# Performance work log

Hardware: AMD Instinct MI355X
Metric: run time of the kernel (lower is better)

## Reference

```python
import jax, jax.numpy as jnp
import numpy as np
import math

D_MODEL = 1024
N_HEADS = 16
HEAD_DIM = D_MODEL // N_HEADS
RANK = 128
SCALE = 1.0 / math.sqrt(HEAD_DIM)


def lowrank(x, u, v, b):
    # y = (x @ u) @ v + b : d_model -> rank -> d_model
    return jnp.einsum('bsd,dr,re->bse', x, u, v) + b


def setup_inputs() -> dict:
    key = jax.random.key(0)
    ks = jax.random.split(key, 16)
    B, S = 2, 2048
    inp = {
        'q': jax.random.normal(ks[0], (B, S, D_MODEL), jnp.float32),
        'k': jax.random.normal(ks[1], (B, S, D_MODEL), jnp.float32),
        'v': jax.random.normal(ks[2], (B, S, D_MODEL), jnp.float32),
        'mask': jnp.ones((B, S), jnp.int32),
    }
    i = 3
    for name in ('q', 'k', 'v', 'out'):
        inp[f'{name}_u'] = jax.random.normal(ks[i], (D_MODEL, RANK), jnp.float32) * 0.02
        inp[f'{name}_v'] = jax.random.normal(ks[i + 1], (RANK, D_MODEL), jnp.float32) * 0.02
        inp[f'{name}_b'] = jnp.zeros((D_MODEL,), jnp.float32)
        i += 2
    return inp


def reference(q, k, v, mask, q_u, q_v, q_b, k_u, k_v, k_b, v_u, v_v, v_b, out_u, out_v, out_b):
    B, S, _ = q.shape
    qh = lowrank(q, q_u, q_v, q_b).reshape(B, S, N_HEADS, HEAD_DIM)
    kh = lowrank(k, k_u, k_v, k_b).reshape(B, S, N_HEADS, HEAD_DIM)
    vh = lowrank(v, v_u, v_v, v_b).reshape(B, S, N_HEADS, HEAD_DIM)
    # scores: [B, H, Sq, Sk]
    scores = jnp.einsum('bqhd,bkhd->bhqk', qh, kh) * SCALE
    scores = jnp.where(mask[:, None, None, :] == 0, -1e9, scores)
    attn = jax.nn.softmax(scores, axis=-1)
    ctx = jnp.einsum('bhqk,bkhd->bqhd', attn, vh).reshape(B, S, D_MODEL)
    return lowrank(ctx, out_u, out_v, out_b)
```

## Files before the change

kernel.cpp:

```cpp
#include <hip/hip_runtime.h>
#include <hip/hip_bf16.h>
#include <stdint.h>

#define DEVI __device__ __forceinline__

typedef __attribute__((ext_vector_type(8))) __bf16 bf16x8;
typedef __attribute__((ext_vector_type(4))) float f32x4;
typedef __attribute__((ext_vector_type(4))) unsigned short us4;

DEVI unsigned short f2bf(float x) {
  union { float f; unsigned u; } v; v.f = x;
  unsigned r = v.u + 0x7FFFu + ((v.u >> 16) & 1u);
  return (unsigned short)(r >> 16);
}

DEVI f32x4 mfma16(bf16x8 a, bf16x8 b, f32x4 c) {
  return __builtin_amdgcn_mfma_f32_16x16x32_bf16(a, b, c, 0, 0, 0);
}

DEVI bf16x8 ld_frag(const unsigned short* tile, int row, int ld, int kbase, int lane) {
  const unsigned short* p = tile + row * ld + kbase + ((lane >> 4) << 2);
  union { bf16x8 f; us4 h[2]; } u;
  u.h[0] = *(const us4*)p;
  u.h[1] = *(const us4*)(p + 16);
  return u.f;
}

struct TP { const float* in[8]; unsigned short* out[8]; };

__global__ __launch_bounds__(256) void wtrans(TP p) {
  const int z = blockIdx.y;
  const int K = (z & 1) ? 128 : 1024;
  const int N = (z & 1) ? 1024 : 128;
  const int i = blockIdx.x * 256 + threadIdx.x;
  const int k = i / N, n = i % N;
  p.out[z][(size_t)n * K + k] = f2bf(p.in[z][i]);
}

struct GP {
  const void* A[3];
  const unsigned short* WT[3];
  const float* bias[3];
  void* C[3];
  float oscale[3];
};

template<bool ABF16, bool OBF16, bool BIAS>
__global__ __launch_bounds__(256)
void gemm_k(GP p, int M, int N, int K) {
  __shared__ unsigned short As[128][36];
  __shared__ unsigned short Ws[64][36];
  const int tid = threadIdx.x, lane = tid & 63, wid = tid >> 6;
  const int z = blockIdx.z;
  const int m0 = blockIdx.x * 128, n0 = blockIdx.y * 64;
  const int wm = (wid >> 1) * 64, wn = (wid & 1) * 32;
  f32x4 acc[4][2] = {};

  const int arow = tid >> 1, aseg = (tid & 1) * 16;
  const int wrow = tid >> 2, wseg = (tid & 3) * 8;
  const float* Af = (const float*)p.A[z];
  const unsigned short* Ab = (const unsigned short*)p.A[z];
  const unsigned short* Wt = p.WT[z];

  for (int k0 = 0; k0 < K; k0 += 32) {
    __syncthreads();
    {
      union { uint4 u[2]; us4 h[4]; unsigned short s[16]; } t;
      if (ABF16) {
        const unsigned short* src = Ab + (size_t)(m0 + arow) * K + k0 + aseg;
        t.u[0] = *(const uint4*)src;
        t.u[1] = *(const uint4*)(src + 8);
      } else {
        const float* src = Af + (size_t)(m0 + arow) * K + k0 + aseg;
        #pragma unroll
        for (int j = 0; j < 16; j += 4) {
          float4 f = *(const float4*)(src + j);
          t.s[j] = f2bf(f.x); t.s[j + 1] = f2bf(f.y);
          t.s[j + 2] = f2bf(f.z); t.s[j + 3] = f2bf(f.w);
        }
      }
      us4* dst = (us4*)&As[arow][aseg];
      dst[0] = t.h[0]; dst[1] = t.h[1]; dst[2] = t.h[2]; dst[3] = t.h[3];
    }
    {
      union { uint4 u; us4 h[2]; } t;
      const unsigned short* src = Wt + (size_t)(n0 + wrow) * K + k0 + wseg;
      t.u = *(const uint4*)src;
      us4* dst = (us4*)&Ws[wrow][wseg];
      dst[0] = t.h[0]; dst[1] = t.h[1];
    }
    __syncthreads();

    bf16x8 af[4], wf[2];
    #pragma unroll
    for (int mi = 0; mi < 4; mi++)
      af[mi] = ld_frag(&As[0][0], wm + mi * 16 + (lane & 15), 36, 0, lane);
    #pragma unroll
    for (int ni = 0; ni < 2; ni++)
      wf[ni] = ld_frag(&Ws[0][0], wn + ni * 16 + (lane & 15), 36, 0, lane);
    #pragma unroll
    for (int mi = 0; mi < 4; mi++)
      #pragma unroll
      for (int ni = 0; ni < 2; ni++)
        acc[mi][ni] = mfma16(af[mi], wf[ni], acc[mi][ni]);
  }

  const float os = p.oscale[z];
  #pragma unroll
  for (int ni = 0; ni < 2; ni++) {
    const int col = n0 + wn + ni * 16 + (lane & 15);
    const float bv = BIAS ? p.bias[z][col] : 0.0f;
    #pragma unroll
    for (int mi = 0; mi < 4; mi++)
      #pragma unroll
      for (int r = 0; r < 4; r++) {
        const int row = m0 + wm + mi * 16 + ((lane >> 4) << 2) + r;
        float vv = (acc[mi][ni][r] + bv) * os;
        if (OBF16) ((unsigned short*)p.C[z])[(size_t)row * N + col] = f2bf(vv);
        else       ((float*)p.C[z])[(size_t)row * N + col] = vv;
      }
  }
}

__global__ __launch_bounds__(256)
void attn_k(const unsigned short* __restrict__ qh, const unsigned short* __restrict__ kh,
            const unsigned short* __restrict__ vh, const int* __restrict__ mask,
            unsigned short* __restrict__ ctx) {
  const int S = 2048, DM = 1024;
  __shared__ unsigned short Ks[64][68];
  __shared__ unsigned short VTs[64][68];
  __shared__ unsigned short Ps[4][32][68];
  __shared__ float mk[64];
  const int tid = threadIdx.x, lane = tid & 63, w = tid >> 6;
  const int b = blockIdx.z, h = blockIdx.y, q0 = blockIdx.x * 128;
  const int qbase = q0 + w * 32;

  bf16x8 qf[2][2];
  #pragma unroll
  for (int mi = 0; mi < 2; mi++)
    #pragma unroll
    for (int kk = 0; kk < 2; kk++) {
      const unsigned short* p = qh + (size_t)(b * S + qbase + mi * 16 + (lane & 15)) * DM
                                + h * 64 + kk * 32 + ((lane >> 4) << 2);
      union { bf16x8 f; us4 h4[2]; } u;
      u.h4[0] = *(const us4*)p;
      u.h4[1] = *(const us4*)(p + 16);
      qf[mi][kk] = u.f;
    }

  float mrow[2][4], lrow[2][4];
  f32x4 acc[2][4] = {};
  #pragma unroll
  for (int mi = 0; mi < 2; mi++)
    #pragma unroll
    for (int r = 0; r < 4; r++) { mrow[mi][r] = -1e30f; lrow[mi][r] = 0.f; }

  const int srow = tid >> 2, sseg = (tid & 3) * 16;

  for (int kv0 = 0; kv0 < S; kv0 += 64) {
    __syncthreads();
    {
      union { uint4 u[2]; us4 h[4]; unsigned short s[16]; } tk, tv;
      const unsigned short* ksrc = kh + (size_t)(b * S + kv0 + srow) * DM + h * 64 + sseg;
      tk.u[0] = *(const uint4*)ksrc; tk.u[1] = *(const uint4*)(ksrc + 8);
      us4* kd = (us4*)&Ks[srow][sseg];
      kd[0] = tk.h[0]; kd[1] = tk.h[1]; kd[2] = tk.h[2]; kd[3] = tk.h[3];
      const unsigned short* vsrc = vh + (size_t)(b * S + kv0 + srow) * DM + h * 64 + sseg;
      tv.u[0] = *(const uint4*)vsrc; tv.u[1] = *(const uint4*)(vsrc + 8);
      #pragma unroll
      for (int j = 0; j < 16; j++) VTs[sseg + j][srow] = tv.s[j];
      if (tid < 64) mk[tid] = (mask[b * S + kv0 + tid] == 0) ? -1e9f : 0.0f;
    }
    __syncthreads();

    f32x4 sc[2][4];
    #pragma unroll
    for (int ni = 0; ni < 4; ni++) {
      bf16x8 kf0 = ld_frag(&Ks[0][0], ni * 16 + (lane & 15), 68, 0, lane);
      bf16x8 kf1 = ld_frag(&Ks[0][0], ni * 16 + (lane & 15), 68, 32, lane);
      #pragma unroll
      for (int mi = 0; mi < 2; mi++) {
        f32x4 zz = {0.f, 0.f, 0.f, 0.f};
        zz = mfma16(qf[mi][0], kf0, zz);
        zz = mfma16(qf[mi][1], kf1, zz);
        sc[mi][ni] = zz;
      }
    }
    #pragma unroll
    for (int mi = 0; mi < 2; mi++)
      #pragma unroll
      for (int ni = 0; ni < 4; ni++) {
        float ma = mk[ni * 16 + (lane & 15)];
        sc[mi][ni] += ma;
      }

    #pragma unroll
    for (int mi = 0; mi < 2; mi++)
      #pragma unroll
      for (int r = 0; r < 4; r++) {
        float tm = fmaxf(fmaxf(sc[mi][0][r], sc[mi][1][r]), fmaxf(sc[mi][2][r], sc[mi][3][r]));
        tm = fmaxf(tm, __shfl_xor(tm, 1));
        tm = fmaxf(tm, __shfl_xor(tm, 2));
        tm = fmaxf(tm, __shfl_xor(tm, 4));
        tm = fmaxf(tm, __shfl_xor(tm, 8));
        float mnew = fmaxf(mrow[mi][r], tm);
        float alpha = __expf(mrow[mi][r] - mnew);
        mrow[mi][r] = mnew;
        float rs = 0.f;
        #pragma unroll
        for (int ni = 0; ni < 4; ni++) {
          float e = __expf(sc[mi][ni][r] - mnew);
          sc[mi][ni][r] = e;
          rs += e;
        }
        rs += __shfl_xor(rs, 1);
        rs += __shfl_xor(rs, 2);
        rs += __shfl_xor(rs, 4);
        rs += __shfl_xor(rs, 8);
        lrow[mi][r] = lrow[mi][r] * alpha + rs;
        #pragma unroll
        for (int di = 0; di < 4; di++) acc[mi][di][r] *= alpha;
      }

    #pragma unroll
    for (int mi = 0; mi < 2; mi++)
      #pragma unroll
      for (int ni = 0; ni < 4; ni++)
        #pragma unroll
        for (int r = 0; r < 4; r++)
          Ps[w][mi * 16 + ((lane >> 4) << 2) + r][ni * 16 + (lane & 15)] = f2bf(sc[mi][ni][r]);

    #pragma unroll
    for (int kk = 0; kk < 2; kk++) {
      bf16x8 pa0 = ld_frag(&Ps[w][0][0], 0 * 16 + (lane & 15), 68, kk * 32, lane);
      bf16x8 pa1 = ld_frag(&Ps[w][0][0], 1 * 16 + (lane & 15), 68, kk * 32, lane);
      #pragma unroll
      for (int di = 0; di < 4; di++) {
        bf16x8 vb = ld_frag(&VTs[0][0], di * 16 + (lane & 15), 68, kk * 32, lane);
        acc[0][di] = mfma16(pa0, vb, acc[0][di]);
        acc[1][di] = mfma16(pa1, vb, acc[1][di]);
      }
    }
  }

  #pragma unroll
  for (int mi = 0; mi < 2; mi++)
    #pragma unroll
    for (int di = 0; di < 4; di++)
      #pragma unroll
      for (int r = 0; r < 4; r++) {
        const int row = qbase + mi * 16 + ((lane >> 4) << 2) + r;
        float o = acc[mi][di][r] / lrow[mi][r];
        ctx[(size_t)(b * S + row) * DM + h * 64 + di * 16 + (lane & 15)] = f2bf(o);
      }
}

extern "C" void kernel_launch(void* const* d_in, const int* in_sizes, int n_in,
                              void* d_out, int out_size, void* d_ws, size_t ws_size,
                              hipStream_t stream) {
  const float* q = (const float*)d_in[0];
  const float* k = (const float*)d_in[1];
  const float* v = (const float*)d_in[2];
  const int* mask = (const int*)d_in[3];
  const float* wu[4] = {(const float*)d_in[4], (const float*)d_in[7],
                        (const float*)d_in[10], (const float*)d_in[13]};
  const float* wv[4] = {(const float*)d_in[5], (const float*)d_in[8],
                        (const float*)d_in[11], (const float*)d_in[14]};
  const float* wb[4] = {(const float*)d_in[6], (const float*)d_in[9],
                        (const float*)d_in[12], (const float*)d_in[15]};

  char* ws = (char*)d_ws;
  unsigned short* WT  = (unsigned short*)ws;
  unsigned short* T0  = (unsigned short*)(ws + 2097152);
  unsigned short* T1  = T0 + 524288;
  unsigned short* T2  = T1 + 524288;
  unsigned short* QH  = (unsigned short*)(ws + 2097152 + 3145728);
  unsigned short* KH  = QH + 4194304;
  unsigned short* VH  = KH + 4194304;
  unsigned short* CTX = VH + 4194304;

  TP tp;
  for (int i = 0; i < 4; i++) { tp.in[2 * i] = wu[i]; tp.in[2 * i + 1] = wv[i]; }
  for (int i = 0; i < 8; i++) tp.out[i] = WT + (size_t)i * 131072;
  wtrans<<<dim3(512, 8), 256, 0, stream>>>(tp);

  const float SCALE = 0.125f;

  GP g1 = {};
  g1.A[0] = q; g1.A[1] = k; g1.A[2] = v;
  g1.WT[0] = tp.out[0]; g1.WT[1] = tp.out[2]; g1.WT[2] = tp.out[4];
  g1.C[0] = T0; g1.C[1] = T1; g1.C[2] = T2;
  g1.oscale[0] = g1.oscale[1] = g1.oscale[2] = 1.f;
  gemm_k<false, true, false><<<dim3(32, 2, 3), 256, 0, stream>>>(g1, 4096, 128, 1024);

  GP g2 = {};
  g2.A[0] = T0; g2.A[1] = T1; g2.A[2] = T2;
  g2.WT[0] = tp.out[1]; g2.WT[1] = tp.out[3]; g2.WT[2] = tp.out[5];
  g2.bias[0] = wb[0]; g2.bias[1] = wb[1]; g2.bias[2] = wb[2];
  g2.C[0] = QH; g2.C[1] = KH; g2.C[2] = VH;
  g2.oscale[0] = SCALE; g2.oscale[1] = 1.f; g2.oscale[2] = 1.f;
  gemm_k<true, true, true><<<dim3(32, 16, 3), 256, 0, stream>>>(g2, 4096, 1024, 128);

  attn_k<<<dim3(16, 16, 2), 256, 0, stream>>>(QH, KH, VH, mask, CTX);

  GP g3 = {};
  g3.A[0] = CTX; g3.WT[0] = tp.out[6]; g3.C[0] = T0; g3.oscale[0] = 1.f;
  gemm_k<true, true, false><<<dim3(32, 2, 1), 256, 0, stream>>>(g3, 4096, 128, 1024);

  GP g4 = {};
  g4.A[0] = T0; g4.WT[0] = tp.out[7]; g4.bias[0] = wb[3];
  g4.C[0] = d_out; g4.oscale[0] = 1.f;
  gemm_k<true, false, true><<<dim3(32, 16, 1), 256, 0, stream>>>(g4, 4096, 1024, 128);
}
```

Before: 319.0 us.

## Compute transposed attention scores to keep P in registers, tile weight transpose

The attention kernel now computes S^T = K·Q^T, so each lane holds a column of scores for one query. The softmax reduction then needs only two cross-lane shuffles, and the probabilities can be packed straight into MFMA B-operand fragments. This removes the per-warp shared-memory round trip for P and its extra LDS traffic. The output is also written with vectorized 4-element stores, the weight transpose uses a 32x32 shared-memory tile for coalesced reads and writes, and f2bf uses the native bf16 conversion.

New measurement: 269.3 us. 15.6% less time.

```diff
diff --git a/kernel.cpp b/kernel.cpp
--- a/kernel.cpp
+++ b/kernel.cpp
@@ -9,9 +9,9 @@
 typedef __attribute__((ext_vector_type(4))) unsigned short us4;
 
 DEVI unsigned short f2bf(float x) {
-  union { float f; unsigned u; } v; v.f = x;
-  unsigned r = v.u + 0x7FFFu + ((v.u >> 16) & 1u);
-  return (unsigned short)(r >> 16);
+  union { __bf16 b; unsigned short s; } u;
+  u.b = (__bf16)x;
+  return u.s;
 }
 
 DEVI f32x4 mfma16(bf16x8 a, bf16x8 b, f32x4 c) {
@@ -28,13 +28,22 @@
 
 struct TP { const float* in[8]; unsigned short* out[8]; };
 
-__global__ __launch_bounds__(256) void wtrans(TP p) {
+__global__ __launch_bounds__(256) void wtrans2(TP p) {
   const int z = blockIdx.y;
-  const int K = (z & 1) ? 128 : 1024;
-  const int N = (z & 1) ? 1024 : 128;
-  const int i = blockIdx.x * 256 + threadIdx.x;
-  const int k = i / N, n = i % N;
-  p.out[z][(size_t)n * K + k] = f2bf(p.in[z][i]);
+  const int R = (z & 1) ? 128 : 1024;
+  const int C = (z & 1) ? 1024 : 128;
+  __shared__ unsigned short T[32][33];
+  const int tilesC = C >> 5;
+  const int tr0 = (blockIdx.x / tilesC) << 5;
+  const int tc0 = (blockIdx.x % tilesC) << 5;
+  const int tx = threadIdx.x & 31, ty = threadIdx.x >> 5;
+  #pragma unroll
+  for (int j = 0; j < 4; j++)
+    T[ty + j * 8][tx] = f2bf(p.in[z][(size_t)(tr0 + ty + j * 8) * C + tc0 + tx]);
+  __syncthreads();
+  #pragma unroll
+  for (int j = 0; j < 4; j++)
+    p.out[z][(size_t)(tc0 + ty + j * 8) * R + tr0 + tx] = T[tx][ty + j * 8];
 }
 
 struct GP {
@@ -123,37 +132,35 @@
 }
 
 __global__ __launch_bounds__(256)
-void attn_k(const unsigned short* __restrict__ qh, const unsigned short* __restrict__ kh,
-            const unsigned short* __restrict__ vh, const int* __restrict__ mask,
-            unsigned short* __restrict__ ctx) {
+void attn_k2(const unsigned short* __restrict__ qh, const unsigned short* __restrict__ kh,
+             const unsigned short* __restrict__ vh, const int* __restrict__ mask,
+             unsigned short* __restrict__ ctx) {
   const int S = 2048, DM = 1024;
   __shared__ unsigned short Ks[64][68];
   __shared__ unsigned short VTs[64][68];
-  __shared__ unsigned short Ps[4][32][68];
-  __shared__ float mk[64];
+  __shared__ alignas(16) float mkadd[64];
   const int tid = threadIdx.x, lane = tid & 63, w = tid >> 6;
   const int b = blockIdx.z, h = blockIdx.y, q0 = blockIdx.x * 128;
   const int qbase = q0 + w * 32;
+  const int lg4 = (lane >> 4) << 2, l15 = lane & 15;
 
   bf16x8 qf[2][2];
   #pragma unroll
-  for (int mi = 0; mi < 2; mi++)
+  for (int ni = 0; ni < 2; ni++)
     #pragma unroll
     for (int kk = 0; kk < 2; kk++) {
-      const unsigned short* p = qh + (size_t)(b * S + qbase + mi * 16 + (lane & 15)) * DM
-                                + h * 64 + kk * 32 + ((lane >> 4) << 2);
+      const unsigned short* p = qh + (size_t)(b * S + qbase + ni * 16 + l15) * DM
+                                + h * 64 + kk * 32 + lg4;
       union { bf16x8 f; us4 h4[2]; } u;
       u.h4[0] = *(const us4*)p;
       u.h4[1] = *(const us4*)(p + 16);
-      qf[mi][kk] = u.f;
-    }
-
-  float mrow[2][4], lrow[2][4];
-  f32x4 acc[2][4] = {};
-  #pragma unroll
-  for (int mi = 0; mi < 2; mi++)
-    #pragma unroll
-    for (int r = 0; r < 4; r++) { mrow[mi][r] = -1e30f; lrow[mi][r] = 0.f; }
+      qf[ni][kk] = u.f;
+    }
+
+  float mrow[2], lrow[2];
+  f32x4 acc_o[4][2] = {};
+  mrow[0] = mrow[1] = -1e30f;
+  lrow[0] = lrow[1] = 0.f;
 
   const int srow = tid >> 2, sseg = (tid & 3) * 16;
 
@@ -169,90 +176,93 @@
       tv.u[0] = *(const uint4*)vsrc; tv.u[1] = *(const uint4*)(vsrc + 8);
       #pragma unroll
       for (int j = 0; j < 16; j++) VTs[sseg + j][srow] = tv.s[j];
-      if (tid < 64) mk[tid] = (mask[b * S + kv0 + tid] == 0) ? -1e9f : 0.0f;
+      if (tid < 64) mkadd[tid] = (mask[b * S + kv0 + tid] == 0) ? -1e9f : 0.0f;
     }
     __syncthreads();
 
-    f32x4 sc[2][4];
-    #pragma unroll
-    for (int ni = 0; ni < 4; ni++) {
-      bf16x8 kf0 = ld_frag(&Ks[0][0], ni * 16 + (lane & 15), 68, 0, lane);
-      bf16x8 kf1 = ld_frag(&Ks[0][0], ni * 16 + (lane & 15), 68, 32, lane);
-      #pragma unroll
-      for (int mi = 0; mi < 2; mi++) {
+    f32x4 sc[4][2];
+    #pragma unroll
+    for (int mi = 0; mi < 4; mi++) {
+      bf16x8 kf0 = ld_frag(&Ks[0][0], mi * 16 + l15, 68, 0, lane);
+      bf16x8 kf1 = ld_frag(&Ks[0][0], mi * 16 + l15, 68, 32, lane);
+      #pragma unroll
+      for (int ni = 0; ni < 2; ni++) {
         f32x4 zz = {0.f, 0.f, 0.f, 0.f};
-        zz = mfma16(qf[mi][0], kf0, zz);
-        zz = mfma16(qf[mi][1], kf1, zz);
+        zz = mfma16(kf0, qf[ni][0], zz);
+        zz = mfma16(kf1, qf[ni][1], zz);
         sc[mi][ni] = zz;
       }
     }
     #pragma unroll
-    for (int mi = 0; mi < 2; mi++)
-      #pragma unroll
-      for (int ni = 0; ni < 4; ni++) {
-        float ma = mk[ni * 16 + (lane & 15)];
-        sc[mi][ni] += ma;
-      }
-
-    #pragma unroll
-    for (int mi = 0; mi < 2; mi++)
-      #pragma unroll
-      for (int r = 0; r < 4; r++) {
-        float tm = fmaxf(fmaxf(sc[mi][0][r], sc[mi][1][r]), fmaxf(sc[mi][2][r], sc[mi][3][r]));
-        tm = fmaxf(tm, __shfl_xor(tm, 1));
-        tm = fmaxf(tm, __shfl_xor(tm, 2));
-        tm = fmaxf(tm, __shfl_xor(tm, 4));
-        tm = fmaxf(tm, __shfl_xor(tm, 8));
-        float mnew = fmaxf(mrow[mi][r], tm);
-        float alpha = __expf(mrow[mi][r] - mnew);
-        mrow[mi][r] = mnew;
-        float rs = 0.f;
+    for (int mi = 0; mi < 4; mi++) {
+      f32x4 mv = *(const f32x4*)&mkadd[mi * 16 + lg4];
+      #pragma unroll
+      for (int ni = 0; ni < 2; ni++) sc[mi][ni] += mv;
+    }
+
+    #pragma unroll
+    for (int ni = 0; ni < 2; ni++) {
+      float pm = sc[0][ni][0];
+      #pragma unroll
+      for (int mi = 0; mi < 4; mi++)
         #pragma unroll
-        for (int ni = 0; ni < 4; ni++) {
+        for (int r = 0; r < 4; r++) pm = fmaxf(pm, sc[mi][ni][r]);
+      pm = fmaxf(pm, __shfl_xor(pm, 16));
+      pm = fmaxf(pm, __shfl_xor(pm, 32));
+      const float mnew = fmaxf(mrow[ni], pm);
+      const float alpha = __expf(mrow[ni] - mnew);
+      mrow[ni] = mnew;
+      float rs = 0.f;
+      #pragma unroll
+      for (int mi = 0; mi < 4; mi++)
+        #pragma unroll
+        for (int r = 0; r < 4; r++) {
           float e = __expf(sc[mi][ni][r] - mnew);
           sc[mi][ni][r] = e;
           rs += e;
         }
-        rs += __shfl_xor(rs, 1);
-        rs += __shfl_xor(rs, 2);
-        rs += __shfl_xor(rs, 4);
-        rs += __shfl_xor(rs, 8);
-        lrow[mi][r] = lrow[mi][r] * alpha + rs;
+      rs += __shfl_xor(rs, 16);
+      rs += __shfl_xor(rs, 32);
+      lrow[ni] = lrow[ni] * alpha + rs;
+      #pragma unroll
+      for (int mi = 0; mi < 4; mi++) acc_o[mi][ni] *= alpha;
+    }
+
+    bf16x8 pb[2][2];
+    #pragma unroll
+    for (int kc = 0; kc < 2; kc++)
+      #pragma unroll
+      for (int ni = 0; ni < 2; ni++) {
+        bf16x8 f;
         #pragma unroll
-        for (int di = 0; di < 4; di++) acc[mi][di][r] *= alpha;
-      }
-
-    #pragma unroll
-    for (int mi = 0; mi < 2; mi++)
-      #pragma unroll
-      for (int ni = 0; ni < 4; ni++)
-        #pragma unroll
-        for (int r = 0; r < 4; r++)
-          Ps[w][mi * 16 + ((lane >> 4) << 2) + r][ni * 16 + (lane & 15)] = f2bf(sc[mi][ni][r]);
-
-    #pragma unroll
-    for (int kk = 0; kk < 2; kk++) {
-      bf16x8 pa0 = ld_frag(&Ps[w][0][0], 0 * 16 + (lane & 15), 68, kk * 32, lane);
-      bf16x8 pa1 = ld_frag(&Ps[w][0][0], 1 * 16 + (lane & 15), 68, kk * 32, lane);
-      #pragma unroll
-      for (int di = 0; di < 4; di++) {
-        bf16x8 vb = ld_frag(&VTs[0][0], di * 16 + (lane & 15), 68, kk * 32, lane);
-        acc[0][di] = mfma16(pa0, vb, acc[0][di]);
-        acc[1][di] = mfma16(pa1, vb, acc[1][di]);
+        for (int e = 0; e < 8; e++)
+          f[e] = (__bf16)sc[2 * kc + (e >> 2)][ni][e & 3];
+        pb[kc][ni] = f;
+      }
+
+    #pragma unroll
+    for (int kc = 0; kc < 2; kc++) {
+      #pragma unroll
+      for (int mi = 0; mi < 4; mi++) {
+        bf16x8 va = ld_frag(&VTs[0][0], mi * 16 + l15, 68, kc * 32, lane);
+        acc_o[mi][0] = mfma16(va, pb[kc][0], acc_o[mi][0]);
+        acc_o[mi][1] = mfma16(va, pb[kc][1], acc_o[mi][1]);
       }
     }
   }
 
   #pragma unroll
-  for (int mi = 0; mi < 2; mi++)
-    #pragma unroll
-    for (int di = 0; di < 4; di++)
-      #pragma unroll
-      for (int r = 0; r < 4; r++) {
-        const int row = qbase + mi * 16 + ((lane >> 4) << 2) + r;
-        float o = acc[mi][di][r] / lrow[mi][r];
-        ctx[(size_t)(b * S + row) * DM + h * 64 + di * 16 + (lane & 15)] = f2bf(o);
-      }
+  for (int ni = 0; ni < 2; ni++) {
+    const float rinv = 1.0f / lrow[ni];
+    const size_t rowoff = (size_t)(b * S + qbase + ni * 16 + l15) * DM + h * 64;
+    #pragma unroll
+    for (int mi = 0; mi < 4; mi++) {
+      us4 o;
+      #pragma unroll
+      for (int r = 0; r < 4; r++) o[r] = f2bf(acc_o[mi][ni][r] * rinv);
+      *(us4*)(ctx + rowoff + mi * 16 + lg4) = o;
+    }
+  }
 }
 
 extern "C" void kernel_launch(void* const* d_in, const int* in_sizes, int n_in,
@@ -282,7 +292,7 @@
   TP tp;
   for (int i = 0; i < 4; i++) { tp.in[2 * i] = wu[i]; tp.in[2 * i + 1] = wv[i]; }
   for (int i = 0; i < 8; i++) tp.out[i] = WT + (size_t)i * 131072;
-  wtrans<<<dim3(512, 8), 256, 0, stream>>>(tp);
+  wtrans2<<<dim3(128, 8), 256, 0, stream>>>(tp);
 
   const float SCALE = 0.125f;
 
@@ -301,7 +311,7 @@
   g2.oscale[0] = SCALE; g2.oscale[1] = 1.f; g2.oscale[2] = 1.f;
   gemm_k<true, true, true><<<dim3(32, 16, 3), 256, 0, stream>>>(g2, 4096, 1024, 128);
 
-  attn_k<<<dim3(16, 16, 2), 256, 0, stream>>>(QH, KH, VH, mask, CTX);
+  attn_k2<<<dim3(16, 16, 2), 256, 0, stream>>>(QH, KH, VH, mask, CTX);
 
   GP g3 = {};
   g3.A[0] = CTX; g3.WT[0] = tp.out[6]; g3.C[0] = T0; g3.oscale[0] = 1.f;
```
